# Kernel tuning notes

Measured on AMD Instinct MI355X. Metric: run time of the kernel, lower is better.

## Reference

```python
import jax, jax.numpy as jnp
import numpy as np

B, S, N = 1024, 64, 256
ODE_UNFOLDS = 12
EPS = 1e-8
ELAPSED_TIME = 1.0

def _uniform(key, shape, lo, hi):
    return jax.random.uniform(key, shape, jnp.float32, lo, hi)

def setup_inputs() -> dict:
    key = jax.random.key(0)
    ks = jax.random.split(key, 16)
    return {
        "inputs": jax.random.normal(ks[0], (B, S), jnp.float32),
        "state": jax.random.normal(ks[1], (B, N), jnp.float32),
        "gleak": _uniform(ks[2], (N,), 0.001, 1.0),
        "vleak": _uniform(ks[3], (N,), -0.2, 0.2),
        "cm": _uniform(ks[4], (N,), 0.4, 0.6),
        "w": _uniform(ks[5], (N, N), 0.001, 1.0),
        "sigma": _uniform(ks[6], (N, N), 3.0, 8.0),
        "mu": _uniform(ks[7], (N, N), 0.3, 0.8),
        "erev": jnp.where(jax.random.bernoulli(ks[8], 0.5, (N, N)), 1.0, -1.0).astype(jnp.float32),
        "sensory_w": _uniform(ks[9], (S, N), 0.001, 1.0),
        "sensory_sigma": _uniform(ks[10], (S, N), 3.0, 8.0),
        "sensory_mu": _uniform(ks[11], (S, N), 0.3, 0.8),
        "sensory_erev": jnp.where(jax.random.bernoulli(ks[12], 0.5, (S, N)), 1.0, -1.0).astype(jnp.float32),
        "sparsity_mask": jax.random.bernoulli(ks[13], 0.5, (N, N)).astype(jnp.float32),
        "sensory_sparsity_mask": jax.random.bernoulli(ks[14], 0.5, (S, N)).astype(jnp.float32),
    }

def _sig(v_pre, mu, sigma):
    # v_pre: [B, pre] -> [B, pre, 1]; mu/sigma: [pre, post] -> broadcast to [B, pre, post]
    return jax.nn.sigmoid(sigma[None] * (v_pre[:, :, None] - mu[None]))

def reference(inputs, state, gleak, vleak, cm, w, sigma, mu, erev,
              sensory_w, sensory_sigma, sensory_mu, sensory_erev,
              sparsity_mask, sensory_sparsity_mask):
    # sensory pre-activation (computed once): [B, S, N]
    sensory_act = jax.nn.softplus(sensory_w) * _sig(inputs, sensory_mu, sensory_sigma)
    sensory_act = sensory_act * sensory_sparsity_mask
    w_num_sensory = jnp.sum(sensory_act * sensory_erev, axis=1)  # [B, N]
    w_den_sensory = jnp.sum(sensory_act, axis=1)                 # [B, N]

    cm_t = jax.nn.softplus(cm) / (ELAPSED_TIME / ODE_UNFOLDS)    # [N]
    w_param = jax.nn.softplus(w)                                 # [N, N]
    gleak_sp = jax.nn.softplus(gleak)                            # [N]

    def step(v_pre, _):
        w_act = w_param * _sig(v_pre, mu, sigma) * sparsity_mask  # [B, N, N]
        w_num = jnp.sum(w_act * erev, axis=1) + w_num_sensory     # [B, N]
        w_den = jnp.sum(w_act, axis=1) + w_den_sensory            # [B, N]
        numerator = cm_t * v_pre + gleak_sp * vleak + w_num
        denominator = cm_t + gleak_sp + w_den
        return numerator / (denominator + EPS), None

    v_pre, _ = jax.lax.scan(step, state, None, length=ODE_UNFOLDS)
    return v_pre
```

## Files before the change

kernel.cpp:

```cpp
#include <hip/hip_runtime.h>
#include <math.h>

#define B_TOT   1024
#define S_DIM   64
#define N_DIM   256
#define UNFOLDS 12
#define EPSF    1e-8f
#define L2E     1.4426950408889634f
#define KMAX    256

typedef unsigned short u16x8 __attribute__((ext_vector_type(8)));

#if defined(__has_builtin)
#  if __has_builtin(__builtin_amdgcn_exp2f)
#    define FEXP2(x) __builtin_amdgcn_exp2f(x)
#  endif
#  if __has_builtin(__builtin_amdgcn_rcpf)
#    define FRCP(x) __builtin_amdgcn_rcpf(x)
#  endif
#endif
#ifndef FEXP2
__device__ __forceinline__ float __fexp2_asm(float x){ float r; asm("v_exp_f32 %0, %1" : "=v"(r) : "v"(x)); return r; }
#  define FEXP2(x) __fexp2_asm(x)
#endif
#ifndef FRCP
__device__ __forceinline__ float __frcp_asm(float x){ float r; asm("v_rcp_f32 %0, %1" : "=v"(r) : "v"(x)); return r; }
#  define FRCP(x) __frcp_asm(x)
#endif

__device__ __forceinline__ float softplus_f(float x) {
    return log1pf(expf(x));
}

__global__ void ltc_precompute_s(const float* __restrict__ gleak, const float* __restrict__ vleak,
                                 const float* __restrict__ cm,
                                 const float* __restrict__ sw,    const float* __restrict__ ssig,
                                 const float* __restrict__ smu,   const float* __restrict__ serev,
                                 const float* __restrict__ smask,
                                 float4* __restrict__ s4, float4* __restrict__ pj,
                                 int* __restrict__ umax)
{
    const int idx = blockIdx.x * blockDim.x + threadIdx.x;
    if (idx < S_DIM * N_DIM) {
        float we = softplus_f(sw[idx]) * smask[idx];
        float sg = ssig[idx];
        float4 o;
        o.x = -L2E * sg;
        o.y =  L2E * sg * smu[idx];
        o.z =  we;
        o.w =  we * serev[idx];
        s4[idx] = o;
    }
    if (idx < N_DIM) {
        float g = softplus_f(gleak[idx]);
        float4 o;
        o.x = softplus_f(cm[idx]) * (float)UNFOLDS;
        o.y = g;
        o.z = g * vleak[idx];
        o.w = 0.0f;
        pj[idx] = o;
    }
    if (idx == 0) *umax = 0;
}

__global__ __launch_bounds__(256)
void ltc_compact(const float* __restrict__ w,    const float* __restrict__ sigma,
                 const float* __restrict__ mu,   const float* __restrict__ erev,
                 const float* __restrict__ mask,
                 float4* __restrict__ pc, unsigned short* __restrict__ pidxT,
                 int* __restrict__ umax)
{
    const int j = blockIdx.x;
    const int i = threadIdx.x;
    const int idx = i * N_DIM + j;

    const float mk = mask[idx];
    const bool live = mk > 0.0f;
    float we = softplus_f(w[idx]) * mk;
    float sg = sigma[idx];
    float4 o;
    o.x = -L2E * sg;
    o.y =  L2E * sg * mu[idx];
    o.z =  we;
    o.w =  we * erev[idx];

    const int lane = i & 63, wv = i >> 6;
    const unsigned long long ball = __ballot(live);
    const int lpre = __popcll(ball & ((1ull << lane) - 1ull));
    __shared__ int wcnt[4];
    if (lane == 0) wcnt[wv] = __popcll(ball);
    __syncthreads();
    int base = 0;
    #pragma unroll
    for (int ww = 0; ww < 4; ++ww) base += (ww < wv) ? wcnt[ww] : 0;
    const int total = wcnt[0] + wcnt[1] + wcnt[2] + wcnt[3];

    if (live) {
        const int pos = base + lpre;
        pc[pos * N_DIM + j] = o;
        pidxT[j * KMAX + pos] = (unsigned short)(i << 4);
    }
    for (int k = total + i; k < KMAX; k += 256) {
        pc[k * N_DIM + j] = make_float4(0.f, 0.f, 0.f, 0.f);
        pidxT[j * KMAX + k] = 0;
    }
    if (i == 0) atomicMax(umax, total);
}

#define LTC_BODY(UU, OFF)                                                   \
    {                                                                       \
        const float4 p  = pr[(t + UU) * N_DIM];                             \
        const float4 vv = *(const float4*)((const char*)v4 + (int)(OFF));   \
        float e0 = FEXP2(fmaf(p.x, vv.x, p.y));                             \
        float e1 = FEXP2(fmaf(p.x, vv.y, p.y));                             \
        float e2 = FEXP2(fmaf(p.x, vv.z, p.y));                             \
        float e3 = FEXP2(fmaf(p.x, vv.w, p.y));                             \
        float r0 = FRCP(1.0f + e0);                                         \
        float r1 = FRCP(1.0f + e1);                                         \
        float r2 = FRCP(1.0f + e2);                                         \
        float r3 = FRCP(1.0f + e3);                                         \
        m0 = fmaf(p.w, r0, m0); d0 = fmaf(p.z, r0, d0);                     \
        m1 = fmaf(p.w, r1, m1); d1 = fmaf(p.z, r1, d1);                     \
        m2 = fmaf(p.w, r2, m2); d2 = fmaf(p.z, r2, d2);                     \
        m3 = fmaf(p.w, r3, m3); d3 = fmaf(p.z, r3, d3);                     \
    }

__global__ __launch_bounds__(1024, 2)
void ltc_main(const float* __restrict__ inputs, const float* __restrict__ state,
              const float4* __restrict__ pc, const unsigned short* __restrict__ pidxT,
              const int* __restrict__ umax,
              const float4* __restrict__ s4, const float4* __restrict__ pj,
              float* __restrict__ out)
{
    __shared__ float4 v4[N_DIM];
    __shared__ float4 pnum[4][N_DIM];
    __shared__ float4 pden[4][N_DIM];
    __shared__ float  in_lds[4][S_DIM];

    const int tid = threadIdx.x;
    const int j   = tid & (N_DIM - 1);
    const int q   = tid >> 8;
    const int b0  = blockIdx.x << 2;

    ((float*)v4)[(j << 2) + q] = state[(b0 + q) * N_DIM + j];
    if (tid < 4 * S_DIM) in_lds[tid >> 6][tid & 63] = inputs[b0 * S_DIM + tid];

    const float4 c = pj[j];
    const float cmt = c.x, gl = c.y, glv = c.z;
    const float cg  = cmt + gl + EPSF;

    const int Ucnt = *umax;
    const int U    = (Ucnt + 31) & ~31;
    const int U4   = U >> 2;
    __syncthreads();

    float n0 = 0.f, n1 = 0.f, n2 = 0.f, n3 = 0.f;
    float d0s = 0.f, d1s = 0.f, d2s = 0.f, d3s = 0.f;
    {
        const float4* __restrict__ sr = s4 + (q << 4) * N_DIM + j;
        const int sbase = q << 4;
        #pragma unroll 4
        for (int s = 0; s < 16; ++s) {
            const float4 p = sr[s * N_DIM];
            float e0 = FEXP2(fmaf(p.x, in_lds[0][sbase + s], p.y));
            float e1 = FEXP2(fmaf(p.x, in_lds[1][sbase + s], p.y));
            float e2 = FEXP2(fmaf(p.x, in_lds[2][sbase + s], p.y));
            float e3 = FEXP2(fmaf(p.x, in_lds[3][sbase + s], p.y));
            float r0 = FRCP(1.0f + e0);
            float r1 = FRCP(1.0f + e1);
            float r2 = FRCP(1.0f + e2);
            float r3 = FRCP(1.0f + e3);
            n0 = fmaf(p.w, r0, n0); d0s = fmaf(p.z, r0, d0s);
            n1 = fmaf(p.w, r1, n1); d1s = fmaf(p.z, r1, d1s);
            n2 = fmaf(p.w, r2, n2); d2s = fmaf(p.z, r2, d2s);
            n3 = fmaf(p.w, r3, n3); d3s = fmaf(p.z, r3, d3s);
        }
    }
    pnum[q][j] = make_float4(n0, n1, n2, n3);
    pden[q][j] = make_float4(d0s, d1s, d2s, d3s);
    __syncthreads();

    float4 sn = make_float4(0.f, 0.f, 0.f, 0.f);
    float4 sd = make_float4(0.f, 0.f, 0.f, 0.f);
    #pragma unroll
    for (int qq = 0; qq < 4; ++qq) {
        const float4 a = pnum[qq][j], b = pden[qq][j];
        sn.x += a.x; sn.y += a.y; sn.z += a.z; sn.w += a.w;
        sd.x += b.x; sd.y += b.y; sd.z += b.z; sd.w += b.w;
    }
    __syncthreads();

    const float4*         __restrict__ pr  = pc    + (q * U4) * N_DIM + j;
    const unsigned short* __restrict__ pi0 = pidxT + j * KMAX + q * U4;

    #pragma unroll 1
    for (int step = 0; step < UNFOLDS; ++step) {
        float m0 = 0.f, m1 = 0.f, m2 = 0.f, m3 = 0.f;
        float d0 = 0.f, d1 = 0.f, d2 = 0.f, d3 = 0.f;

        for (int t = 0; t < U4; t += 8) {
            const u16x8 ix = *(const u16x8*)(pi0 + t);
            LTC_BODY(0, ix.s0)
            LTC_BODY(1, ix.s1)
            LTC_BODY(2, ix.s2)
            LTC_BODY(3, ix.s3)
            LTC_BODY(4, ix.s4)
            LTC_BODY(5, ix.s5)
            LTC_BODY(6, ix.s6)
            LTC_BODY(7, ix.s7)
        }

        const float4 vo = v4[j];
        pnum[q][j] = make_float4(m0, m1, m2, m3);
        pden[q][j] = make_float4(d0, d1, d2, d3);
        __syncthreads();

        float4 tn = sn, td = sd;
        #pragma unroll
        for (int qq = 0; qq < 4; ++qq) {
            const float4 a = pnum[qq][j], b = pden[qq][j];
            tn.x += a.x; tn.y += a.y; tn.z += a.z; tn.w += a.w;
            td.x += b.x; td.y += b.y; td.z += b.z; td.w += b.w;
        }
        float4 vn;
        vn.x = (fmaf(cmt, vo.x, glv) + tn.x) * FRCP(cg + td.x);
        vn.y = (fmaf(cmt, vo.y, glv) + tn.y) * FRCP(cg + td.y);
        vn.z = (fmaf(cmt, vo.z, glv) + tn.z) * FRCP(cg + td.z);
        vn.w = (fmaf(cmt, vo.w, glv) + tn.w) * FRCP(cg + td.w);
        v4[j] = vn;
        __syncthreads();
    }

    out[(b0 + q) * N_DIM + j] = ((const float*)v4)[(j << 2) + q];
}

extern "C" void kernel_launch(void* const* d_in, const int* in_sizes, int n_in,
                              void* d_out, int out_size, void* d_ws, size_t ws_size,
                              hipStream_t stream)
{
    const float* inputs = (const float*)d_in[0];
    const float* state  = (const float*)d_in[1];
    const float* gleak  = (const float*)d_in[2];
    const float* vleak  = (const float*)d_in[3];
    const float* cm     = (const float*)d_in[4];
    const float* w      = (const float*)d_in[5];
    const float* sigma  = (const float*)d_in[6];
    const float* mu     = (const float*)d_in[7];
    const float* erev   = (const float*)d_in[8];
    const float* sw     = (const float*)d_in[9];
    const float* ssig   = (const float*)d_in[10];
    const float* smu    = (const float*)d_in[11];
    const float* serev  = (const float*)d_in[12];
    const float* mask   = (const float*)d_in[13];
    const float* smask  = (const float*)d_in[14];

    float4* s4 = (float4*)d_ws;
    float4* pj = s4 + S_DIM * N_DIM;
    float4* pc = pj + N_DIM;
    unsigned short* pidxT = (unsigned short*)(pc + KMAX * N_DIM);
    int* umax = (int*)(pidxT + N_DIM * KMAX);

    ltc_precompute_s<<<(S_DIM * N_DIM + 255) / 256, 256, 0, stream>>>(
        gleak, vleak, cm, sw, ssig, smu, serev, smask, s4, pj, umax);

    ltc_compact<<<N_DIM, 256, 0, stream>>>(w, sigma, mu, erev, mask, pc, pidxT, umax);

    ltc_main<<<B_TOT / 4, 1024, 0, stream>>>(inputs, state, pc, pidxT, umax,
                                             s4, pj, (float*)d_out);
}
```

Before: 164.2 us.

## Batch sigmoid reciprocals, use per-wave loop bounds, two-batch blocks with ping-pong state

Replaces four reciprocals per group with one shared reciprocal plus multiplies, clamping exp2 so the product of four denominators cannot overflow. The batch tile drops from four rows per 1024-thread block to two rows per 512-thread block, and state moves to a double-buffered layout. Compacted neighbour indices become byte-wide in a column-major layout, and each 64-column wave group gets its own maximum live count so padded iterations shrink. The aim is to cut transcendental work and padding, at the cost of reloading each parameter float4 for only two batch rows instead of four.

```diff
diff --git a/kernel.cpp b/kernel.cpp
--- a/kernel.cpp
+++ b/kernel.cpp
@@ -8,8 +8,7 @@
 #define EPSF    1e-8f
 #define L2E     1.4426950408889634f
 #define KMAX    256
-
-typedef unsigned short u16x8 __attribute__((ext_vector_type(8)));
+#define ECLAMP  1073741824.0f
 
 #if defined(__has_builtin)
 #  if __has_builtin(__builtin_amdgcn_exp2f)
@@ -32,13 +31,36 @@
     return log1pf(expf(x));
 }
 
+#define QUAD_BODY(p0, p1, vA0, vB0, vA1, vB1, mA, dA, mB, dB)               \
+    {                                                                       \
+        float t0 = fmaf(p0.x, vA0, p0.y);                                   \
+        float t1 = fmaf(p0.x, vB0, p0.y);                                   \
+        float t2 = fmaf(p1.x, vA1, p1.y);                                   \
+        float t3 = fmaf(p1.x, vB1, p1.y);                                   \
+        float e0 = fminf(FEXP2(t0), ECLAMP);                                \
+        float e1 = fminf(FEXP2(t1), ECLAMP);                                \
+        float e2 = fminf(FEXP2(t2), ECLAMP);                                \
+        float e3 = fminf(FEXP2(t3), ECLAMP);                                \
+        float a0 = 1.0f + e0, a1 = 1.0f + e1;                               \
+        float a2 = 1.0f + e2, a3 = 1.0f + e3;                               \
+        float b01 = a0 * a1, b23 = a2 * a3;                                 \
+        float ip  = FRCP(b01 * b23);                                        \
+        float ip01 = b23 * ip, ip23 = b01 * ip;                             \
+        float r0 = a1 * ip01, r1 = a0 * ip01;                               \
+        float r2 = a3 * ip23, r3 = a2 * ip23;                               \
+        mA = fmaf(p0.w, r0, mA); dA = fmaf(p0.z, r0, dA);                   \
+        mB = fmaf(p0.w, r1, mB); dB = fmaf(p0.z, r1, dB);                   \
+        mA = fmaf(p1.w, r2, mA); dA = fmaf(p1.z, r2, dA);                   \
+        mB = fmaf(p1.w, r3, mB); dB = fmaf(p1.z, r3, dB);                   \
+    }
+
 __global__ void ltc_precompute_s(const float* __restrict__ gleak, const float* __restrict__ vleak,
                                  const float* __restrict__ cm,
                                  const float* __restrict__ sw,    const float* __restrict__ ssig,
                                  const float* __restrict__ smu,   const float* __restrict__ serev,
                                  const float* __restrict__ smask,
                                  float4* __restrict__ s4, float4* __restrict__ pj,
-                                 int* __restrict__ umax)
+                                 int* __restrict__ wmax)
 {
     const int idx = blockIdx.x * blockDim.x + threadIdx.x;
     if (idx < S_DIM * N_DIM) {
@@ -60,15 +82,15 @@
         o.w = 0.0f;
         pj[idx] = o;
     }
-    if (idx == 0) *umax = 0;
+    if (idx < 4) wmax[idx] = 0;
 }
 
 __global__ __launch_bounds__(256)
 void ltc_compact(const float* __restrict__ w,    const float* __restrict__ sigma,
                  const float* __restrict__ mu,   const float* __restrict__ erev,
                  const float* __restrict__ mask,
-                 float4* __restrict__ pc, unsigned short* __restrict__ pidxT,
-                 int* __restrict__ umax)
+                 float4* __restrict__ pc, unsigned char* __restrict__ pidxK,
+                 int* __restrict__ wmax)
 {
     const int j = blockIdx.x;
     const int i = threadIdx.x;
@@ -98,140 +120,107 @@
     if (live) {
         const int pos = base + lpre;
         pc[pos * N_DIM + j] = o;
-        pidxT[j * KMAX + pos] = (unsigned short)(i << 4);
+        pidxK[pos * N_DIM + j] = (unsigned char)i;
     }
     for (int k = total + i; k < KMAX; k += 256) {
         pc[k * N_DIM + j] = make_float4(0.f, 0.f, 0.f, 0.f);
-        pidxT[j * KMAX + k] = 0;
-    }
-    if (i == 0) atomicMax(umax, total);
-}
-
-#define LTC_BODY(UU, OFF)                                                   \
-    {                                                                       \
-        const float4 p  = pr[(t + UU) * N_DIM];                             \
-        const float4 vv = *(const float4*)((const char*)v4 + (int)(OFF));   \
-        float e0 = FEXP2(fmaf(p.x, vv.x, p.y));                             \
-        float e1 = FEXP2(fmaf(p.x, vv.y, p.y));                             \
-        float e2 = FEXP2(fmaf(p.x, vv.z, p.y));                             \
-        float e3 = FEXP2(fmaf(p.x, vv.w, p.y));                             \
-        float r0 = FRCP(1.0f + e0);                                         \
-        float r1 = FRCP(1.0f + e1);                                         \
-        float r2 = FRCP(1.0f + e2);                                         \
-        float r3 = FRCP(1.0f + e3);                                         \
-        m0 = fmaf(p.w, r0, m0); d0 = fmaf(p.z, r0, d0);                     \
-        m1 = fmaf(p.w, r1, m1); d1 = fmaf(p.z, r1, d1);                     \
-        m2 = fmaf(p.w, r2, m2); d2 = fmaf(p.z, r2, d2);                     \
-        m3 = fmaf(p.w, r3, m3); d3 = fmaf(p.z, r3, d3);                     \
-    }
-
-__global__ __launch_bounds__(1024, 2)
+        pidxK[k * N_DIM + j] = 0;
+    }
+    if (i == 0) atomicMax(&wmax[j >> 6], total);
+}
+
+__global__ __launch_bounds__(512, 4)
 void ltc_main(const float* __restrict__ inputs, const float* __restrict__ state,
-              const float4* __restrict__ pc, const unsigned short* __restrict__ pidxT,
-              const int* __restrict__ umax,
+              const float4* __restrict__ pc, const unsigned char* __restrict__ pidxK,
+              const int* __restrict__ wmax,
               const float4* __restrict__ s4, const float4* __restrict__ pj,
               float* __restrict__ out)
 {
-    __shared__ float4 v4[N_DIM];
-    __shared__ float4 pnum[4][N_DIM];
-    __shared__ float4 pden[4][N_DIM];
-    __shared__ float  in_lds[4][S_DIM];
+    __shared__ float  vbuf[2][2][N_DIM];
+    __shared__ float4 pS[2][N_DIM];
+    __shared__ float  in_lds[2][S_DIM];
 
     const int tid = threadIdx.x;
     const int j   = tid & (N_DIM - 1);
     const int q   = tid >> 8;
-    const int b0  = blockIdx.x << 2;
-
-    ((float*)v4)[(j << 2) + q] = state[(b0 + q) * N_DIM + j];
-    if (tid < 4 * S_DIM) in_lds[tid >> 6][tid & 63] = inputs[b0 * S_DIM + tid];
+    const int b0  = blockIdx.x << 1;
+
+    {
+        const int b = tid >> 8, i = tid & (N_DIM - 1);
+        vbuf[0][b][i] = state[(b0 + b) * N_DIM + i];
+    }
+    if (tid < 2 * S_DIM) in_lds[tid >> 6][tid & 63] = inputs[b0 * S_DIM + tid];
 
     const float4 c = pj[j];
     const float cmt = c.x, gl = c.y, glv = c.z;
     const float cg  = cmt + gl + EPSF;
 
-    const int Ucnt = *umax;
-    const int U    = (Ucnt + 31) & ~31;
-    const int U4   = U >> 2;
-    __syncthreads();
-
-    float n0 = 0.f, n1 = 0.f, n2 = 0.f, n3 = 0.f;
-    float d0s = 0.f, d1s = 0.f, d2s = 0.f, d3s = 0.f;
+    const int wl   = wmax[j >> 6];
+    const int U2w  = (((wl + 7) & ~7) >> 1);
+    __syncthreads();
+
+    float snA = 0.f, sdA = 0.f, snB = 0.f, sdB = 0.f;
     {
-        const float4* __restrict__ sr = s4 + (q << 4) * N_DIM + j;
-        const int sbase = q << 4;
+        const float4* __restrict__ sr = s4 + (q << 5) * N_DIM + j;
+        const int sb = q << 5;
         #pragma unroll 4
-        for (int s = 0; s < 16; ++s) {
-            const float4 p = sr[s * N_DIM];
-            float e0 = FEXP2(fmaf(p.x, in_lds[0][sbase + s], p.y));
-            float e1 = FEXP2(fmaf(p.x, in_lds[1][sbase + s], p.y));
-            float e2 = FEXP2(fmaf(p.x, in_lds[2][sbase + s], p.y));
-            float e3 = FEXP2(fmaf(p.x, in_lds[3][sbase + s], p.y));
-            float r0 = FRCP(1.0f + e0);
-            float r1 = FRCP(1.0f + e1);
-            float r2 = FRCP(1.0f + e2);
-            float r3 = FRCP(1.0f + e3);
-            n0 = fmaf(p.w, r0, n0); d0s = fmaf(p.z, r0, d0s);
-            n1 = fmaf(p.w, r1, n1); d1s = fmaf(p.z, r1, d1s);
-            n2 = fmaf(p.w, r2, n2); d2s = fmaf(p.z, r2, d2s);
-            n3 = fmaf(p.w, r3, n3); d3s = fmaf(p.z, r3, d3s);
+        for (int s = 0; s < 32; s += 2) {
+            const float4 p0 = sr[s * N_DIM];
+            const float4 p1 = sr[(s + 1) * N_DIM];
+            const float iA0 = in_lds[0][sb + s],     iB0 = in_lds[1][sb + s];
+            const float iA1 = in_lds[0][sb + s + 1], iB1 = in_lds[1][sb + s + 1];
+            QUAD_BODY(p0, p1, iA0, iB0, iA1, iB1, snA, sdA, snB, sdB)
         }
     }
-    pnum[q][j] = make_float4(n0, n1, n2, n3);
-    pden[q][j] = make_float4(d0s, d1s, d2s, d3s);
-    __syncthreads();
-
-    float4 sn = make_float4(0.f, 0.f, 0.f, 0.f);
-    float4 sd = make_float4(0.f, 0.f, 0.f, 0.f);
-    #pragma unroll
-    for (int qq = 0; qq < 4; ++qq) {
-        const float4 a = pnum[qq][j], b = pden[qq][j];
-        sn.x += a.x; sn.y += a.y; sn.z += a.z; sn.w += a.w;
-        sd.x += b.x; sd.y += b.y; sd.z += b.z; sd.w += b.w;
-    }
-    __syncthreads();
-
-    const float4*         __restrict__ pr  = pc    + (q * U4) * N_DIM + j;
-    const unsigned short* __restrict__ pi0 = pidxT + j * KMAX + q * U4;
+    pS[q][j] = make_float4(snA, sdA, snB, sdB);
+    __syncthreads();
+
+    float4 sen, sed;
+    {
+        const float4 a0 = pS[0][j], a1 = pS[1][j];
+        sen = make_float4(a0.x + a1.x, a0.z + a1.z, 0.f, 0.f);
+        sed = make_float4(a0.y + a1.y, a0.w + a1.w, 0.f, 0.f);
+    }
+    __syncthreads();
+
+    const float4*        __restrict__ pr0 = pc    + (q * U2w) * N_DIM + j;
+    const unsigned char* __restrict__ pi0 = pidxK + (q * U2w) * N_DIM + j;
+
+    float* va = &vbuf[0][0][0];
+    float* vb = &vbuf[1][0][0];
 
     #pragma unroll 1
     for (int step = 0; step < UNFOLDS; ++step) {
-        float m0 = 0.f, m1 = 0.f, m2 = 0.f, m3 = 0.f;
-        float d0 = 0.f, d1 = 0.f, d2 = 0.f, d3 = 0.f;
-
-        for (int t = 0; t < U4; t += 8) {
-            const u16x8 ix = *(const u16x8*)(pi0 + t);
-            LTC_BODY(0, ix.s0)
-            LTC_BODY(1, ix.s1)
-            LTC_BODY(2, ix.s2)
-            LTC_BODY(3, ix.s3)
-            LTC_BODY(4, ix.s4)
-            LTC_BODY(5, ix.s5)
-            LTC_BODY(6, ix.s6)
-            LTC_BODY(7, ix.s7)
+        float mA = 0.f, dA = 0.f, mB = 0.f, dB = 0.f;
+
+        #pragma unroll 2
+        for (int t = 0; t < U2w; t += 2) {
+            const float4 p0 = pr0[t * N_DIM];
+            const float4 p1 = pr0[(t + 1) * N_DIM];
+            const int i0 = (int)pi0[t * N_DIM];
+            const int i1 = (int)pi0[(t + 1) * N_DIM];
+            const float vA0 = va[i0], vB0 = va[N_DIM + i0];
+            const float vA1 = va[i1], vB1 = va[N_DIM + i1];
+            QUAD_BODY(p0, p1, vA0, vB0, vA1, vB1, mA, dA, mB, dB)
         }
 
-        const float4 vo = v4[j];
-        pnum[q][j] = make_float4(m0, m1, m2, m3);
-        pden[q][j] = make_float4(d0, d1, d2, d3);
+        const float voA = va[j], voB = va[N_DIM + j];
+        pS[q][j] = make_float4(mA, dA, mB, dB);
         __syncthreads();
 
-        float4 tn = sn, td = sd;
-        #pragma unroll
-        for (int qq = 0; qq < 4; ++qq) {
-            const float4 a = pnum[qq][j], b = pden[qq][j];
-            tn.x += a.x; tn.y += a.y; tn.z += a.z; tn.w += a.w;
-            td.x += b.x; td.y += b.y; td.z += b.z; td.w += b.w;
-        }
-        float4 vn;
-        vn.x = (fmaf(cmt, vo.x, glv) + tn.x) * FRCP(cg + td.x);
-        vn.y = (fmaf(cmt, vo.y, glv) + tn.y) * FRCP(cg + td.y);
-        vn.z = (fmaf(cmt, vo.z, glv) + tn.z) * FRCP(cg + td.z);
-        vn.w = (fmaf(cmt, vo.w, glv) + tn.w) * FRCP(cg + td.w);
-        v4[j] = vn;
+        const float4 a0 = pS[0][j], a1 = pS[1][j];
+        const float tnA = sen.x + a0.x + a1.x;
+        const float tdA = sed.x + a0.y + a1.y;
+        const float tnB = sen.y + a0.z + a1.z;
+        const float tdB = sed.y + a0.w + a1.w;
+        vb[j]         = (fmaf(cmt, voA, glv) + tnA) * FRCP(cg + tdA);
+        vb[N_DIM + j] = (fmaf(cmt, voB, glv) + tnB) * FRCP(cg + tdB);
         __syncthreads();
-    }
-
-    out[(b0 + q) * N_DIM + j] = ((const float*)v4)[(j << 2) + q];
+
+        float* tmp = va; va = vb; vb = tmp;
+    }
+
+    out[(b0 + q) * N_DIM + j] = va[q * N_DIM + j];
 }
 
 extern "C" void kernel_launch(void* const* d_in, const int* in_sizes, int n_in,
@@ -257,14 +246,14 @@
     float4* s4 = (float4*)d_ws;
     float4* pj = s4 + S_DIM * N_DIM;
     float4* pc = pj + N_DIM;
-    unsigned short* pidxT = (unsigned short*)(pc + KMAX * N_DIM);
-    int* umax = (int*)(pidxT + N_DIM * KMAX);
+    unsigned char* pidxK = (unsigned char*)(pc + KMAX * N_DIM);
+    int* wmax = (int*)(pidxK + KMAX * N_DIM);
 
     ltc_precompute_s<<<(S_DIM * N_DIM + 255) / 256, 256, 0, stream>>>(
-        gleak, vleak, cm, sw, ssig, smu, serev, smask, s4, pj, umax);
-
-    ltc_compact<<<N_DIM, 256, 0, stream>>>(w, sigma, mu, erev, mask, pc, pidxT, umax);
-
-    ltc_main<<<B_TOT / 4, 1024, 0, stream>>>(inputs, state, pc, pidxT, umax,
-                                             s4, pj, (float*)d_out);
-}
+        gleak, vleak, cm, sw, ssig, smu, serev, smask, s4, pj, wmax);
+
+    ltc_compact<<<N_DIM, 256, 0, stream>>>(w, sigma, mu, erev, mask, pc, pidxK, wmax);
+
+    ltc_main<<<B_TOT / 2, 512, 0, stream>>>(inputs, state, pc, pidxK, wmax,
+                                            s4, pj, (float*)d_out);
+}
```

New measurement: 180.5 us. 1.1x slower.

## Share one reciprocal across four sigmoids and use per-wave loop bounds

Applied to the files above, without the earlier changes.

The four sigmoid reciprocals per weight are replaced by one reciprocal of the product of the four denominators plus a few multiplies, with the exp clamped so the product cannot overflow. The final division in each step gets the same treatment. The compacted pre-synapse index table is transposed to [k][j] so each thread loads one coalesced ushort per iteration instead of a vector of eight. Trip counts now come from a per-wave maximum rather than a global one, so waves with fewer live synapses do less work. This trades transcendental-unit throughput for extra VALU multiplies, adds a small accuracy risk from the clamp, and introduces more scalar loads of the index table.

```diff
diff --git a/kernel.cpp b/kernel.cpp
--- a/kernel.cpp
+++ b/kernel.cpp
@@ -8,8 +8,7 @@
 #define EPSF    1e-8f
 #define L2E     1.4426950408889634f
 #define KMAX    256
-
-typedef unsigned short u16x8 __attribute__((ext_vector_type(8)));
+#define ECLAMP  1073741824.0f
 
 #if defined(__has_builtin)
 #  if __has_builtin(__builtin_amdgcn_exp2f)
@@ -32,13 +31,36 @@
     return log1pf(expf(x));
 }
 
+#define MQUAD(p, v0, v1, v2, v3, m0, d0, m1, d1, m2, d2, m3, d3)            \
+    {                                                                       \
+        float _t0 = fmaf(p.x, v0, p.y);                                     \
+        float _t1 = fmaf(p.x, v1, p.y);                                     \
+        float _t2 = fmaf(p.x, v2, p.y);                                     \
+        float _t3 = fmaf(p.x, v3, p.y);                                     \
+        float _e0 = fminf(FEXP2(_t0), ECLAMP);                              \
+        float _e1 = fminf(FEXP2(_t1), ECLAMP);                              \
+        float _e2 = fminf(FEXP2(_t2), ECLAMP);                              \
+        float _e3 = fminf(FEXP2(_t3), ECLAMP);                              \
+        float _a0 = 1.0f + _e0, _a1 = 1.0f + _e1;                           \
+        float _a2 = 1.0f + _e2, _a3 = 1.0f + _e3;                           \
+        float _b01 = _a0 * _a1, _b23 = _a2 * _a3;                           \
+        float _ip   = FRCP(_b01 * _b23);                                    \
+        float _ip01 = _b23 * _ip, _ip23 = _b01 * _ip;                       \
+        float _r0 = _a1 * _ip01, _r1 = _a0 * _ip01;                         \
+        float _r2 = _a3 * _ip23, _r3 = _a2 * _ip23;                         \
+        m0 = fmaf(p.w, _r0, m0); d0 = fmaf(p.z, _r0, d0);                   \
+        m1 = fmaf(p.w, _r1, m1); d1 = fmaf(p.z, _r1, d1);                   \
+        m2 = fmaf(p.w, _r2, m2); d2 = fmaf(p.z, _r2, d2);                   \
+        m3 = fmaf(p.w, _r3, m3); d3 = fmaf(p.z, _r3, d3);                   \
+    }
+
 __global__ void ltc_precompute_s(const float* __restrict__ gleak, const float* __restrict__ vleak,
                                  const float* __restrict__ cm,
                                  const float* __restrict__ sw,    const float* __restrict__ ssig,
                                  const float* __restrict__ smu,   const float* __restrict__ serev,
                                  const float* __restrict__ smask,
                                  float4* __restrict__ s4, float4* __restrict__ pj,
-                                 int* __restrict__ umax)
+                                 int* __restrict__ wmax)
 {
     const int idx = blockIdx.x * blockDim.x + threadIdx.x;
     if (idx < S_DIM * N_DIM) {
@@ -60,15 +82,15 @@
         o.w = 0.0f;
         pj[idx] = o;
     }
-    if (idx == 0) *umax = 0;
+    if (idx < 4) wmax[idx] = 0;
 }
 
 __global__ __launch_bounds__(256)
 void ltc_compact(const float* __restrict__ w,    const float* __restrict__ sigma,
                  const float* __restrict__ mu,   const float* __restrict__ erev,
                  const float* __restrict__ mask,
-                 float4* __restrict__ pc, unsigned short* __restrict__ pidxT,
-                 int* __restrict__ umax)
+                 float4* __restrict__ pc, unsigned short* __restrict__ pofs,
+                 int* __restrict__ wmax)
 {
     const int j = blockIdx.x;
     const int i = threadIdx.x;
@@ -98,37 +120,19 @@
     if (live) {
         const int pos = base + lpre;
         pc[pos * N_DIM + j] = o;
-        pidxT[j * KMAX + pos] = (unsigned short)(i << 4);
+        pofs[pos * N_DIM + j] = (unsigned short)(i << 4);
     }
     for (int k = total + i; k < KMAX; k += 256) {
         pc[k * N_DIM + j] = make_float4(0.f, 0.f, 0.f, 0.f);
-        pidxT[j * KMAX + k] = 0;
-    }
-    if (i == 0) atomicMax(umax, total);
-}
-
-#define LTC_BODY(UU, OFF)                                                   \
-    {                                                                       \
-        const float4 p  = pr[(t + UU) * N_DIM];                             \
-        const float4 vv = *(const float4*)((const char*)v4 + (int)(OFF));   \
-        float e0 = FEXP2(fmaf(p.x, vv.x, p.y));                             \
-        float e1 = FEXP2(fmaf(p.x, vv.y, p.y));                             \
-        float e2 = FEXP2(fmaf(p.x, vv.z, p.y));                             \
-        float e3 = FEXP2(fmaf(p.x, vv.w, p.y));                             \
-        float r0 = FRCP(1.0f + e0);                                         \
-        float r1 = FRCP(1.0f + e1);                                         \
-        float r2 = FRCP(1.0f + e2);                                         \
-        float r3 = FRCP(1.0f + e3);                                         \
-        m0 = fmaf(p.w, r0, m0); d0 = fmaf(p.z, r0, d0);                     \
-        m1 = fmaf(p.w, r1, m1); d1 = fmaf(p.z, r1, d1);                     \
-        m2 = fmaf(p.w, r2, m2); d2 = fmaf(p.z, r2, d2);                     \
-        m3 = fmaf(p.w, r3, m3); d3 = fmaf(p.z, r3, d3);                     \
-    }
+        pofs[k * N_DIM + j] = 0;
+    }
+    if (i == 0) atomicMax(&wmax[j >> 6], total);
+}
 
 __global__ __launch_bounds__(1024, 2)
 void ltc_main(const float* __restrict__ inputs, const float* __restrict__ state,
-              const float4* __restrict__ pc, const unsigned short* __restrict__ pidxT,
-              const int* __restrict__ umax,
+              const float4* __restrict__ pc, const unsigned short* __restrict__ pofs,
+              const int* __restrict__ wmax,
               const float4* __restrict__ s4, const float4* __restrict__ pj,
               float* __restrict__ out)
 {
@@ -149,35 +153,27 @@
     const float cmt = c.x, gl = c.y, glv = c.z;
     const float cg  = cmt + gl + EPSF;
 
-    const int Ucnt = *umax;
-    const int U    = (Ucnt + 31) & ~31;
-    const int U4   = U >> 2;
+    const int wl  = wmax[j >> 6];
+    const int U4w = ((wl + 31) & ~31) >> 2;
     __syncthreads();
 
     float n0 = 0.f, n1 = 0.f, n2 = 0.f, n3 = 0.f;
-    float d0s = 0.f, d1s = 0.f, d2s = 0.f, d3s = 0.f;
+    float d0 = 0.f, d1 = 0.f, d2 = 0.f, d3 = 0.f;
     {
         const float4* __restrict__ sr = s4 + (q << 4) * N_DIM + j;
-        const int sbase = q << 4;
+        const int sb = q << 4;
         #pragma unroll 4
         for (int s = 0; s < 16; ++s) {
             const float4 p = sr[s * N_DIM];
-            float e0 = FEXP2(fmaf(p.x, in_lds[0][sbase + s], p.y));
-            float e1 = FEXP2(fmaf(p.x, in_lds[1][sbase + s], p.y));
-            float e2 = FEXP2(fmaf(p.x, in_lds[2][sbase + s], p.y));
-            float e3 = FEXP2(fmaf(p.x, in_lds[3][sbase + s], p.y));
-            float r0 = FRCP(1.0f + e0);
-            float r1 = FRCP(1.0f + e1);
-            float r2 = FRCP(1.0f + e2);
-            float r3 = FRCP(1.0f + e3);
-            n0 = fmaf(p.w, r0, n0); d0s = fmaf(p.z, r0, d0s);
-            n1 = fmaf(p.w, r1, n1); d1s = fmaf(p.z, r1, d1s);
-            n2 = fmaf(p.w, r2, n2); d2s = fmaf(p.z, r2, d2s);
-            n3 = fmaf(p.w, r3, n3); d3s = fmaf(p.z, r3, d3s);
+            const float i0 = in_lds[0][sb + s];
+            const float i1 = in_lds[1][sb + s];
+            const float i2 = in_lds[2][sb + s];
+            const float i3 = in_lds[3][sb + s];
+            MQUAD(p, i0, i1, i2, i3, n0, d0, n1, d1, n2, d2, n3, d3)
         }
     }
     pnum[q][j] = make_float4(n0, n1, n2, n3);
-    pden[q][j] = make_float4(d0s, d1s, d2s, d3s);
+    pden[q][j] = make_float4(d0, d1, d2, d3);
     __syncthreads();
 
     float4 sn = make_float4(0.f, 0.f, 0.f, 0.f);
@@ -190,29 +186,25 @@
     }
     __syncthreads();
 
-    const float4*         __restrict__ pr  = pc    + (q * U4) * N_DIM + j;
-    const unsigned short* __restrict__ pi0 = pidxT + j * KMAX + q * U4;
+    const float4*         __restrict__ pr = pc   + (q * U4w) * N_DIM + j;
+    const unsigned short* __restrict__ po = pofs + (q * U4w) * N_DIM + j;
 
     #pragma unroll 1
     for (int step = 0; step < UNFOLDS; ++step) {
         float m0 = 0.f, m1 = 0.f, m2 = 0.f, m3 = 0.f;
-        float d0 = 0.f, d1 = 0.f, d2 = 0.f, d3 = 0.f;
-
-        for (int t = 0; t < U4; t += 8) {
-            const u16x8 ix = *(const u16x8*)(pi0 + t);
-            LTC_BODY(0, ix.s0)
-            LTC_BODY(1, ix.s1)
-            LTC_BODY(2, ix.s2)
-            LTC_BODY(3, ix.s3)
-            LTC_BODY(4, ix.s4)
-            LTC_BODY(5, ix.s5)
-            LTC_BODY(6, ix.s6)
-            LTC_BODY(7, ix.s7)
+        float h0 = 0.f, h1 = 0.f, h2 = 0.f, h3 = 0.f;
+
+        #pragma unroll 8
+        for (int t = 0; t < U4w; ++t) {
+            const float4 p   = pr[t * N_DIM];
+            const int    off = (int)po[t * N_DIM];
+            const float4 vv  = *(const float4*)((const char*)v4 + off);
+            MQUAD(p, vv.x, vv.y, vv.z, vv.w, m0, h0, m1, h1, m2, h2, m3, h3)
         }
 
         const float4 vo = v4[j];
         pnum[q][j] = make_float4(m0, m1, m2, m3);
-        pden[q][j] = make_float4(d0, d1, d2, d3);
+        pden[q][j] = make_float4(h0, h1, h2, h3);
         __syncthreads();
 
         float4 tn = sn, td = sd;
@@ -222,11 +214,16 @@
             tn.x += a.x; tn.y += a.y; tn.z += a.z; tn.w += a.w;
             td.x += b.x; td.y += b.y; td.z += b.z; td.w += b.w;
         }
+        const float g0 = cg + td.x, g1 = cg + td.y;
+        const float g2 = cg + td.z, g3 = cg + td.w;
+        const float b01 = g0 * g1, b23 = g2 * g3;
+        const float ip   = FRCP(b01 * b23);
+        const float ip01 = b23 * ip, ip23 = b01 * ip;
         float4 vn;
-        vn.x = (fmaf(cmt, vo.x, glv) + tn.x) * FRCP(cg + td.x);
-        vn.y = (fmaf(cmt, vo.y, glv) + tn.y) * FRCP(cg + td.y);
-        vn.z = (fmaf(cmt, vo.z, glv) + tn.z) * FRCP(cg + td.z);
-        vn.w = (fmaf(cmt, vo.w, glv) + tn.w) * FRCP(cg + td.w);
+        vn.x = (fmaf(cmt, vo.x, glv) + tn.x) * (g1 * ip01);
+        vn.y = (fmaf(cmt, vo.y, glv) + tn.y) * (g0 * ip01);
+        vn.z = (fmaf(cmt, vo.z, glv) + tn.z) * (g3 * ip23);
+        vn.w = (fmaf(cmt, vo.w, glv) + tn.w) * (g2 * ip23);
         v4[j] = vn;
         __syncthreads();
     }
@@ -257,14 +254,14 @@
     float4* s4 = (float4*)d_ws;
     float4* pj = s4 + S_DIM * N_DIM;
     float4* pc = pj + N_DIM;
-    unsigned short* pidxT = (unsigned short*)(pc + KMAX * N_DIM);
-    int* umax = (int*)(pidxT + N_DIM * KMAX);
+    unsigned short* pofs = (unsigned short*)(pc + KMAX * N_DIM);
+    int* wmax = (int*)(pofs + KMAX * N_DIM);
 
     ltc_precompute_s<<<(S_DIM * N_DIM + 255) / 256, 256, 0, stream>>>(
-        gleak, vleak, cm, sw, ssig, smu, serev, smask, s4, pj, umax);
-
-    ltc_compact<<<N_DIM, 256, 0, stream>>>(w, sigma, mu, erev, mask, pc, pidxT, umax);
-
-    ltc_main<<<B_TOT / 4, 1024, 0, stream>>>(inputs, state, pc, pidxT, umax,
+        gleak, vleak, cm, sw, ssig, smu, serev, smask, s4, pj, wmax);
+
+    ltc_compact<<<N_DIM, 256, 0, stream>>>(w, sigma, mu, erev, mask, pc, pofs, wmax);
+
+    ltc_main<<<B_TOT / 4, 1024, 0, stream>>>(inputs, state, pc, pofs, wmax,
                                              s4, pj, (float*)d_out);
 }
```

New measurement: 158.1 us. -3.7%, faster.
